# Kernel tuning notes

Hardware: AMD Instinct MI355X
Metric: run time of the kernel (lower is better)

Reference implementation:

```python
import jax, jax.numpy as jnp
import numpy as np
from jax import lax

C = 256            # channels
K = 7              # kernel_size
RED = 4            # reduction_ratio
GC = 16            # group_channels
G = C // GC        # groups
PAD = (K - 1) // 2
EPS = 1e-5


def setup_inputs() -> dict:
    key = jax.random.key(0)
    ks = jax.random.split(key, 8)
    B, H, W = 4, 64, 64
    x = jax.random.normal(ks[0], (B, C, H, W), dtype=jnp.float32)
    # conv1: 1x1 conv C -> C/4, then BN (eval-mode running stats), ReLU
    w1 = jax.random.normal(ks[1], (C // RED, C), dtype=jnp.float32) * (1.0 / np.sqrt(C))
    b1 = jnp.zeros((C // RED,), dtype=jnp.float32)
    gamma = jnp.ones((C // RED,), dtype=jnp.float32)
    beta = jnp.zeros((C // RED,), dtype=jnp.float32)
    mean = jax.random.normal(ks[2], (C // RED,), dtype=jnp.float32) * 0.1
    var = jax.random.uniform(ks[3], (C // RED,), dtype=jnp.float32, minval=0.5, maxval=1.5)
    # conv2: 1x1 conv C/4 -> K^2 * G
    w2 = jax.random.normal(ks[4], (K * K * G, C // RED), dtype=jnp.float32) * (1.0 / np.sqrt(C // RED))
    b2 = jnp.zeros((K * K * G,), dtype=jnp.float32)
    return {"x": x, "w1": w1, "b1": b1, "gamma": gamma, "beta": beta,
            "mean": mean, "var": var, "w2": w2, "b2": b2}


def reference(x, w1, b1, gamma, beta, mean, var, w2, b2):
    b, c, h, w = x.shape
    # kernel-generation branch (stride==1, so no avgpool)
    t = jnp.einsum('bchw,oc->bohw', x, w1) + b1[None, :, None, None]
    t = gamma[None, :, None, None] * (t - mean[None, :, None, None]) \
        * lax.rsqrt(var + EPS)[None, :, None, None] + beta[None, :, None, None]
    t = jax.nn.relu(t)
    weight = jnp.einsum('bchw,oc->bohw', t, w2) + b2[None, :, None, None]
    # (b, G, 1, K*K, h, w)
    weight = weight.reshape(b, G, K * K, h, w)[:, :, None]
    # im2col patches: (b, C*K*K, h, w) with channel-major (c, kh, kw) ordering,
    # matching torch.nn.Unfold
    patches = lax.conv_general_dilated_patches(
        x, filter_shape=(K, K), window_strides=(1, 1),
        padding=((PAD, PAD), (PAD, PAD)))
    patches = patches.reshape(b, G, GC, K * K, h, w)
    out = (weight * patches).sum(axis=3).reshape(b, C, h, w)
    return out
```

## Files before the change

### kernel.cpp

```cpp
#include <hip/hip_runtime.h>

#define C_IN 256
#define CR   64
#define G_   16
#define GC_  16
#define K_   7
#define KK   49
#define PAD_ 3
#define H_   64
#define W_   64
#define HW   4096
#define OO   784
#define EPSV 1e-5f
#define WTAPS 13

__global__ __launch_bounds__(256) void prep_kernel(
    const float* __restrict__ w1, const float* __restrict__ b1,
    const float* __restrict__ gamma, const float* __restrict__ beta,
    const float* __restrict__ mean, const float* __restrict__ var,
    const float* __restrict__ w2,
    float* __restrict__ w1t, float* __restrict__ b1f, float* __restrict__ w2t)
{
  int idx = blockIdx.x * 256 + threadIdx.x;
  if (idx < CR * C_IN) {
    int o = idx / C_IN, c = idx % C_IN;
    float s = gamma[o] * rsqrtf(var[o] + EPSV);
    w1t[c * CR + o] = w1[idx] * s;
  }
  if (idx < CR) {
    float s = gamma[idx] * rsqrtf(var[idx] + EPSV);
    b1f[idx] = (b1[idx] - mean[idx]) * s + beta[idx];
  }
  if (idx < OO * CR) {
    int o = idx / CR, c = idx % CR;
    w2t[c * OO + o] = w2[idx];
  }
}

__global__ __launch_bounds__(1024) void conv1_kernel(
    const float* __restrict__ x, const float* __restrict__ w1t,
    const float* __restrict__ b1f, float* __restrict__ t)
{
  const int px = threadIdx.x & 63;
  const int j  = __builtin_amdgcn_readfirstlane(threadIdx.x >> 6);
  const int o0 = j * 4;
  const int hw0 = blockIdx.x * 64;
  const int b   = blockIdx.y;

  const float* xb = x + ((size_t)b * C_IN) * HW + hw0 + px;

  float acc[4] = {0.f, 0.f, 0.f, 0.f};
#pragma unroll 8
  for (int c = 0; c < C_IN; ++c) {
    float xv = xb[(size_t)c * HW];
    float4 wv = *(const float4*)(w1t + c * CR + o0);
    acc[0] = fmaf(xv, wv.x, acc[0]);
    acc[1] = fmaf(xv, wv.y, acc[1]);
    acc[2] = fmaf(xv, wv.z, acc[2]);
    acc[3] = fmaf(xv, wv.w, acc[3]);
  }

  float4 bb = *(const float4*)(b1f + o0);
  float r[4];
  r[0] = fmaxf(acc[0] + bb.x, 0.f);
  r[1] = fmaxf(acc[1] + bb.y, 0.f);
  r[2] = fmaxf(acc[2] + bb.z, 0.f);
  r[3] = fmaxf(acc[3] + bb.w, 0.f);
  *(float4*)(t + ((size_t)(b * HW + hw0 + px)) * CR + o0) = *(float4*)r;
}

__global__ __launch_bounds__(256) void conv2invol_kernel(
    const float* __restrict__ x, const float* __restrict__ t,
    const float* __restrict__ w2t,
    const float* __restrict__ b2, float* __restrict__ out)
{
  __shared__ float wlds[KK * 64];
  const int tid = threadIdx.x;

  const int L     = blockIdx.x;
  const int xcd   = L & 7;
  const int chunk = L >> 3;
  const int g     = chunk >> 5;
  const int pr    = (chunk & 31) + (xcd << 5);
  const int b     = pr >> 6;
  const int row   = pr & 63;

  {
    const int px  = tid & 63;
    const int j   = __builtin_amdgcn_readfirstlane(tid >> 6);
    const int kk0 = j * WTAPS;

    float acc[WTAPS];
#pragma unroll
    for (int i = 0; i < WTAPS; ++i) {
      int kk = kk0 + i; kk = kk < KK ? kk : KK - 1;
      acc[i] = b2[g * KK + kk];
    }

    const float* tb = t + ((size_t)(b * HW + row * W_ + px)) * CR;
#pragma unroll 4
    for (int c0 = 0; c0 < 16; ++c0) {
      float xv[4];
      *(float4*)xv = *(const float4*)(tb + 4 * c0);
#pragma unroll
      for (int cc = 0; cc < 4; ++cc) {
        const float* wr = w2t + (4 * c0 + cc) * OO + g * KK;
#pragma unroll
        for (int i = 0; i < WTAPS; ++i) {
          int kk = kk0 + i; kk = kk < KK ? kk : KK - 1;
          acc[i] = fmaf(xv[cc], wr[kk], acc[i]);
        }
      }
    }
#pragma unroll
    for (int i = 0; i < WTAPS; ++i) {
      int kk = kk0 + i;
      if (kk < KK) wlds[kk * 64 + px] = acc[i];
    }
  }
  __syncthreads();

  const int quad = tid & 15;
  const int gc   = tid >> 4;
  const int w0   = quad * 4;

  float acc4[4] = {0.f, 0.f, 0.f, 0.f};
  const float* xp = x + ((size_t)b * C_IN + g * GC_ + gc) * HW;

#pragma unroll
  for (int kh = 0; kh < K_; ++kh) {
    const int y = row + kh - PAD_;
    if ((unsigned)y < (unsigned)H_) {
      const float* xr = xp + y * W_;
      float win[12];
      float4 zero4 = {0.f, 0.f, 0.f, 0.f};
      *(float4*)&win[0] = (w0 >= 4)  ? *(const float4*)(xr + w0 - 4) : zero4;
      *(float4*)&win[4] = *(const float4*)(xr + w0);
      *(float4*)&win[8] = (w0 <= 56) ? *(const float4*)(xr + w0 + 4) : zero4;
#pragma unroll
      for (int dw = 0; dw < 7; ++dw) {
        float wv[4];
        *(float4*)wv = *(const float4*)&wlds[(kh * 7 + dw) * 64 + w0];
#pragma unroll
        for (int cc = 0; cc < 4; ++cc)
          acc4[cc] = fmaf(wv[cc], win[cc + dw + 1], acc4[cc]);
      }
    }
  }

  float* ob = out + ((size_t)b * C_IN + g * GC_ + gc) * HW + row * W_ + w0;
  *(float4*)ob = *(float4*)acc4;
}

extern "C" void kernel_launch(void* const* d_in, const int* in_sizes, int n_in,
                              void* d_out, int out_size, void* d_ws, size_t ws_size,
                              hipStream_t stream) {
  const float* x     = (const float*)d_in[0];
  const float* w1    = (const float*)d_in[1];
  const float* b1    = (const float*)d_in[2];
  const float* gamma = (const float*)d_in[3];
  const float* beta  = (const float*)d_in[4];
  const float* mean  = (const float*)d_in[5];
  const float* var   = (const float*)d_in[6];
  const float* w2    = (const float*)d_in[7];
  const float* b2    = (const float*)d_in[8];
  float* out = (float*)d_out;
  const int B = in_sizes[0] / (C_IN * HW);

  char* p = (char*)d_ws;
  float* w1t = (float*)p;  p += ((size_t)CR * C_IN * 4 + 255) & ~(size_t)255;
  float* b1f = (float*)p;  p += ((size_t)CR * 4 + 255) & ~(size_t)255;
  float* w2t = (float*)p;  p += ((size_t)OO * CR * 4 + 511) & ~(size_t)255;
  float* t   = (float*)p;

  prep_kernel<<<dim3((OO * CR + 255) / 256), 256, 0, stream>>>(
      w1, b1, gamma, beta, mean, var, w2, w1t, b1f, w2t);

  conv1_kernel<<<dim3(HW / 64, B), 1024, 0, stream>>>(x, w1t, b1f, t);

  conv2invol_kernel<<<dim3(H_ * G_ * B), 256, 0, stream>>>(x, t, w2t, b2, out);
}
```

Baseline: 180.2 us.

## Fuse conv1, conv2 and involution into one per-row kernel with LDS staging

Combines the 1x1 conv, BN/ReLU, kernel-generation conv and involution into a single kernel, one 1024-thread block per (batch,row). The x row is staged in LDS, conv1 output is kept in LDS instead of a global t buffer, and involution weights are generated in four chunks of four groups each. This removes the t round-trip through global memory, the w2 transpose and two launches. The cost is far fewer blocks (B*H=256) with heavy LDS use, and w2 is now read directly in row-major order with per-thread strided loads, which can lower occupancy and parallelism.

New measurement: 196.7 us. +9.2%, slower.

```diff
diff --git a/kernel.cpp b/kernel.cpp
--- a/kernel.cpp
+++ b/kernel.cpp
@@ -12,144 +12,148 @@
 #define HW   4096
 #define OO   784
 #define EPSV 1e-5f
-#define WTAPS 13
+#define NT   13
+#define CHUNK_T 196
 
 __global__ __launch_bounds__(256) void prep_kernel(
     const float* __restrict__ w1, const float* __restrict__ b1,
     const float* __restrict__ gamma, const float* __restrict__ beta,
     const float* __restrict__ mean, const float* __restrict__ var,
-    const float* __restrict__ w2,
-    float* __restrict__ w1t, float* __restrict__ b1f, float* __restrict__ w2t)
+    float* __restrict__ w1t, float* __restrict__ b1f)
 {
   int idx = blockIdx.x * 256 + threadIdx.x;
   if (idx < CR * C_IN) {
-    int o = idx / C_IN, c = idx % C_IN;
+    int c = idx / CR, o = idx % CR;
     float s = gamma[o] * rsqrtf(var[o] + EPSV);
-    w1t[c * CR + o] = w1[idx] * s;
+    w1t[idx] = w1[o * C_IN + c] * s;
   }
   if (idx < CR) {
     float s = gamma[idx] * rsqrtf(var[idx] + EPSV);
     b1f[idx] = (b1[idx] - mean[idx]) * s + beta[idx];
   }
-  if (idx < OO * CR) {
-    int o = idx / CR, c = idx % CR;
-    w2t[c * OO + o] = w2[idx];
-  }
 }
 
-__global__ __launch_bounds__(1024) void conv1_kernel(
+__global__ __launch_bounds__(1024) void fused_kernel(
     const float* __restrict__ x, const float* __restrict__ w1t,
-    const float* __restrict__ b1f, float* __restrict__ t)
-{
-  const int px = threadIdx.x & 63;
-  const int j  = __builtin_amdgcn_readfirstlane(threadIdx.x >> 6);
-  const int o0 = j * 4;
-  const int hw0 = blockIdx.x * 64;
-  const int b   = blockIdx.y;
-
-  const float* xb = x + ((size_t)b * C_IN) * HW + hw0 + px;
-
-  float acc[4] = {0.f, 0.f, 0.f, 0.f};
-#pragma unroll 8
-  for (int c = 0; c < C_IN; ++c) {
-    float xv = xb[(size_t)c * HW];
-    float4 wv = *(const float4*)(w1t + c * CR + o0);
-    acc[0] = fmaf(xv, wv.x, acc[0]);
-    acc[1] = fmaf(xv, wv.y, acc[1]);
-    acc[2] = fmaf(xv, wv.z, acc[2]);
-    acc[3] = fmaf(xv, wv.w, acc[3]);
-  }
-
-  float4 bb = *(const float4*)(b1f + o0);
-  float r[4];
-  r[0] = fmaxf(acc[0] + bb.x, 0.f);
-  r[1] = fmaxf(acc[1] + bb.y, 0.f);
-  r[2] = fmaxf(acc[2] + bb.z, 0.f);
-  r[3] = fmaxf(acc[3] + bb.w, 0.f);
-  *(float4*)(t + ((size_t)(b * HW + hw0 + px)) * CR + o0) = *(float4*)r;
-}
-
-__global__ __launch_bounds__(256) void conv2invol_kernel(
-    const float* __restrict__ x, const float* __restrict__ t,
-    const float* __restrict__ w2t,
+    const float* __restrict__ b1f,
+    const float* __restrict__ w2,
     const float* __restrict__ b2, float* __restrict__ out)
 {
-  __shared__ float wlds[KK * 64];
+  __shared__ float smem[20480];
+  float* xs = smem;
+  float* wl = smem;
+  float* tl = smem + 16384;
   const int tid = threadIdx.x;
 
-  const int L     = blockIdx.x;
-  const int xcd   = L & 7;
-  const int chunk = L >> 3;
-  const int g     = chunk >> 5;
-  const int pr    = (chunk & 31) + (xcd << 5);
-  const int b     = pr >> 6;
-  const int row   = pr & 63;
+  const int L   = blockIdx.x;
+  const int per = gridDim.x >> 3;
+  const int pr  = (L >> 3) + (L & 7) * per;
+  const int b   = pr >> 6, row = pr & 63;
 
   {
-    const int px  = tid & 63;
-    const int j   = __builtin_amdgcn_readfirstlane(tid >> 6);
-    const int kk0 = j * WTAPS;
-
-    float acc[WTAPS];
+    const float* xrow = x + ((size_t)b * C_IN) * HW + row * W_;
+    const int px4 = (tid & 15) * 4;
+    const int c0  = tid >> 4;
 #pragma unroll
-    for (int i = 0; i < WTAPS; ++i) {
-      int kk = kk0 + i; kk = kk < KK ? kk : KK - 1;
-      acc[i] = b2[g * KK + kk];
-    }
-
-    const float* tb = t + ((size_t)(b * HW + row * W_ + px)) * CR;
-#pragma unroll 4
-    for (int c0 = 0; c0 < 16; ++c0) {
-      float xv[4];
-      *(float4*)xv = *(const float4*)(tb + 4 * c0);
-#pragma unroll
-      for (int cc = 0; cc < 4; ++cc) {
-        const float* wr = w2t + (4 * c0 + cc) * OO + g * KK;
-#pragma unroll
-        for (int i = 0; i < WTAPS; ++i) {
-          int kk = kk0 + i; kk = kk < KK ? kk : KK - 1;
-          acc[i] = fmaf(xv[cc], wr[kk], acc[i]);
-        }
-      }
-    }
-#pragma unroll
-    for (int i = 0; i < WTAPS; ++i) {
-      int kk = kk0 + i;
-      if (kk < KK) wlds[kk * 64 + px] = acc[i];
+    for (int r = 0; r < 4; ++r) {
+      int c = c0 + r * 64;
+      *(float4*)(xs + c * 64 + px4) =
+          *(const float4*)(xrow + (size_t)c * HW + px4);
     }
   }
   __syncthreads();
 
-  const int quad = tid & 15;
-  const int gc   = tid >> 4;
-  const int w0   = quad * 4;
+  {
+    const int px = tid & 63;
+    const int j  = __builtin_amdgcn_readfirstlane(tid >> 6);
+    const int o0 = j * 4;
+    float4 bb = *(const float4*)(b1f + o0);
+    float acc[4] = {bb.x, bb.y, bb.z, bb.w};
+#pragma unroll 8
+    for (int c = 0; c < C_IN; ++c) {
+      float xv  = xs[c * 64 + px];
+      float4 wv = *(const float4*)(w1t + c * CR + o0);
+      acc[0] = fmaf(xv, wv.x, acc[0]);
+      acc[1] = fmaf(xv, wv.y, acc[1]);
+      acc[2] = fmaf(xv, wv.z, acc[2]);
+      acc[3] = fmaf(xv, wv.w, acc[3]);
+    }
+#pragma unroll
+    for (int q = 0; q < 4; ++q)
+      tl[(o0 + q) * 64 + px] = fmaxf(acc[q], 0.f);
+  }
+  __syncthreads();
 
-  float acc4[4] = {0.f, 0.f, 0.f, 0.f};
-  const float* xp = x + ((size_t)b * C_IN + g * GC_ + gc) * HW;
+#pragma unroll 1
+  for (int gchunk = 0; gchunk < 4; ++gchunk) {
+    const int oo0 = gchunk * CHUNK_T;
 
+    {
+      const int px = tid & 63;
+      const int j  = __builtin_amdgcn_readfirstlane(tid >> 6);
+      const int t0 = j * NT;
+      float acc[NT];
 #pragma unroll
-  for (int kh = 0; kh < K_; ++kh) {
-    const int y = row + kh - PAD_;
-    if ((unsigned)y < (unsigned)H_) {
-      const float* xr = xp + y * W_;
-      float win[12];
-      float4 zero4 = {0.f, 0.f, 0.f, 0.f};
-      *(float4*)&win[0] = (w0 >= 4)  ? *(const float4*)(xr + w0 - 4) : zero4;
-      *(float4*)&win[4] = *(const float4*)(xr + w0);
-      *(float4*)&win[8] = (w0 <= 56) ? *(const float4*)(xr + w0 + 4) : zero4;
+      for (int i = 0; i < NT; ++i) {
+        int T = t0 + i; T = T < CHUNK_T ? T : CHUNK_T - 1;
+        acc[i] = b2[oo0 + T];
+      }
+#pragma unroll 2
+      for (int c0 = 0; c0 < CR; c0 += 8) {
+        float tr[8];
 #pragma unroll
-      for (int dw = 0; dw < 7; ++dw) {
-        float wv[4];
-        *(float4*)wv = *(const float4*)&wlds[(kh * 7 + dw) * 64 + w0];
+        for (int q = 0; q < 8; ++q) tr[q] = tl[(c0 + q) * 64 + px];
 #pragma unroll
-        for (int cc = 0; cc < 4; ++cc)
-          acc4[cc] = fmaf(wv[cc], win[cc + dw + 1], acc4[cc]);
+        for (int i = 0; i < NT; ++i) {
+          int T = t0 + i; T = T < CHUNK_T ? T : CHUNK_T - 1;
+          const float* wr = w2 + (size_t)(oo0 + T) * CR + c0;
+#pragma unroll
+          for (int q = 0; q < 8; ++q)
+            acc[i] = fmaf(tr[q], wr[q], acc[i]);
+        }
+      }
+#pragma unroll
+      for (int i = 0; i < NT; ++i) {
+        int T = t0 + i;
+        if (T < CHUNK_T) wl[T * 64 + px] = acc[i];
       }
     }
+    __syncthreads();
+
+    {
+      const int quad = tid & 15;
+      const int gc   = (tid >> 4) & 15;
+      const int gl   = __builtin_amdgcn_readfirstlane(tid >> 8);
+      const int ch   = (gchunk * 4 + gl) * GC_ + gc;
+      const int w0   = quad * 4;
+
+      float acc4[4] = {0.f, 0.f, 0.f, 0.f};
+      const float* xp = x + ((size_t)b * C_IN + ch) * HW;
+#pragma unroll
+      for (int kh = 0; kh < K_; ++kh) {
+        const int y = row + kh - PAD_;
+        if ((unsigned)y < (unsigned)H_) {
+          const float* xr = xp + y * W_;
+          float win[12];
+          float4 z4 = {0.f, 0.f, 0.f, 0.f};
+          *(float4*)&win[0] = (w0 >= 4)  ? *(const float4*)(xr + w0 - 4) : z4;
+          *(float4*)&win[4] = *(const float4*)(xr + w0);
+          *(float4*)&win[8] = (w0 <= 56) ? *(const float4*)(xr + w0 + 4) : z4;
+#pragma unroll
+          for (int dw = 0; dw < K_; ++dw) {
+            float wv[4];
+            *(float4*)wv = *(const float4*)(wl + (gl * KK + kh * 7 + dw) * 64 + w0);
+#pragma unroll
+            for (int cc = 0; cc < 4; ++cc)
+              acc4[cc] = fmaf(wv[cc], win[cc + dw + 1], acc4[cc]);
+          }
+        }
+      }
+      *(float4*)(out + ((size_t)b * C_IN + ch) * HW + row * W_ + w0) =
+          *(float4*)acc4;
+    }
+    __syncthreads();
   }
-
-  float* ob = out + ((size_t)b * C_IN + g * GC_ + gc) * HW + row * W_ + w0;
-  *(float4*)ob = *(float4*)acc4;
 }
 
 extern "C" void kernel_launch(void* const* d_in, const int* in_sizes, int n_in,
@@ -169,14 +173,10 @@
 
   char* p = (char*)d_ws;
   float* w1t = (float*)p;  p += ((size_t)CR * C_IN * 4 + 255) & ~(size_t)255;
-  float* b1f = (float*)p;  p += ((size_t)CR * 4 + 255) & ~(size_t)255;
-  float* w2t = (float*)p;  p += ((size_t)OO * CR * 4 + 511) & ~(size_t)255;
-  float* t   = (float*)p;
+  float* b1f = (float*)p;
 
-  prep_kernel<<<dim3((OO * CR + 255) / 256), 256, 0, stream>>>(
-      w1, b1, gamma, beta, mean, var, w2, w1t, b1f, w2t);
+  prep_kernel<<<dim3((CR * C_IN + 255) / 256), 256, 0, stream>>>(
+      w1, b1, gamma, beta, mean, var, w1t, b1f);
 
-  conv1_kernel<<<dim3(HW / 64, B), 1024, 0, stream>>>(x, w1t, b1f, t);
-
-  conv2invol_kernel<<<dim3(H_ * G_ * B), 256, 0, stream>>>(x, t, w2t, b2, out);
+  fused_kernel<<<dim3(B * H_), 1024, 0, stream>>>(x, w1t, b1f, w2, b2, out);
 }
```
